# Kernel tuning notes

Hardware: AMD Instinct MI355X
Metric: run time of the kernel (lower is better)

## Reference

```python
import jax, jax.numpy as jnp
import numpy as np

B = 8          # events per batch
NPB = 8192     # points per event (equal counts -> Nmax = NPB)
N = B * NPB
FEAT = 6
K = 128        # max_tokens
TOK = 768      # token_dim
KNN = 16       # k_neighbors
MLP_DIMS = [FEAT, 256, 512, 768, TOK]


def setup_inputs() -> dict:
    key = jax.random.key(0)
    ks = jax.random.split(key, 20)
    coords = jax.random.normal(ks[0], (N, 3), jnp.float32) * 5.0
    features = jax.random.normal(ks[1], (N, FEAT), jnp.float32)
    times = jax.random.uniform(ks[2], (N, 1), jnp.float32)
    # equal-sized, sorted batch ids (8192 points per event)
    batch_ids = jnp.repeat(jnp.arange(B, dtype=jnp.int32), NPB)
    inp = {"coords": coords, "features": features, "batch_ids": batch_ids, "times": times}
    # per-point MLP: 6 -> 256 -> 512 -> 768 -> 768 (last Linear has no ReLU)
    ki = 3
    for i in range(4):
        din, dout = MLP_DIMS[i], MLP_DIMS[i + 1]
        inp[f"W{i+1}"] = jax.random.normal(ks[ki], (din, dout), jnp.float32) / np.sqrt(din); ki += 1
        inp[f"b{i+1}"] = jnp.zeros((dout,), jnp.float32)
    # neighborhood MLP: 768 -> 768 -> 768
    inp["Wn1"] = jax.random.normal(ks[ki], (TOK, TOK), jnp.float32) / np.sqrt(TOK); ki += 1
    inp["bn1"] = jnp.zeros((TOK,), jnp.float32)
    inp["Wn2"] = jax.random.normal(ks[ki], (TOK, TOK), jnp.float32) / np.sqrt(TOK); ki += 1
    inp["bn2"] = jnp.zeros((TOK,), jnp.float32)
    return inp


def _forward(coords, features, batch_ids, times,
             W1, b1, W2, b2, W3, b3, W4, b4, Wn1, bn1, Wn2, bn2):
    INF = jnp.float32(jnp.inf)
    points4 = jnp.concatenate([coords[:, :3], times], axis=-1)  # [N,4] (x,y,z,t)
    # per-point MLP
    h = jax.nn.relu(features @ W1 + b1)
    h = jax.nn.relu(h @ W2 + b2)
    h = jax.nn.relu(h @ W3 + b3)
    feats = h @ W4 + b4                                          # [N,TOK]
    # ---- pack flat -> padded [B, NPB, *] ----
    counts = jnp.bincount(batch_ids, length=B)                   # [B]
    offsets = jnp.cumsum(counts) - counts
    pos = jnp.arange(N) - offsets[batch_ids]
    P = jnp.zeros((B, NPB, 4), points4.dtype).at[batch_ids, pos].set(points4)
    Fp = jnp.zeros((B, NPB, TOK), feats.dtype).at[batch_ids, pos].set(feats)
    valid = jnp.arange(NPB)[None, :] < counts[:, None]           # [B,NPB]
    # ---- small path: take first K points sorted by time ----
    tsort = jnp.where(valid, P[..., 3], INF)
    sorted_idx = jnp.argsort(tsort, axis=1)[:, :K]               # K <= NPB
    tokens_small = jnp.take_along_axis(Fp, sorted_idx[..., None], axis=1)
    cents_small = jnp.take_along_axis(P, sorted_idx[..., None], axis=1)
    masks_small = jnp.arange(K)[None, :] < jnp.minimum(counts, K)[:, None]
    tokens_small = tokens_small * masks_small[..., None]
    cents_small = cents_small * masks_small[..., None]
    # ---- batched FPS over 4D points ----
    min_d0 = jnp.where(valid, INF, 0.0)
    norms = jnp.where(valid, jnp.sum(P * P, axis=-1), -INF)
    first = jnp.argmax(norms, axis=1)                            # farthest-from-origin start
    barange = jnp.arange(B)
    def fps_step(carry, _):
        min_d, last = carry
        c = P[barange, last]                                     # [B,4]
        d = jnp.sum((P - c[:, None, :]) ** 2, axis=-1)
        d = jnp.where(valid, d, INF)
        min_d = jnp.minimum(min_d, d)
        return (min_d, jnp.argmax(min_d, axis=1)), last
    _, idx_seq = jax.lax.scan(fps_step, (min_d0, first), None, length=K)
    fps_idx = idx_seq.T                                          # [B,K]
    validK = jnp.arange(K)[None, :] < jnp.minimum(counts, K)[:, None]
    cents_large = jnp.take_along_axis(P, fps_idx[..., None], axis=1)  # [B,K,4]
    # ---- kNN pooling around centroids ----
    diff = cents_large[:, :, None, :] - P[:, None, :, :]         # [B,K,NPB,4]
    dists = jnp.sum(diff * diff, axis=-1)                        # [B,K,NPB]
    dists = jnp.where(valid[:, None, :], dists, INF)
    k_g = min(KNN, NPB)
    _, knn_idx = jax.lax.top_k(-dists, k_g)                      # smallest-k -> [B,K,k]
    knn_valid = jnp.take_along_axis(jnp.broadcast_to(valid[:, None, :], (B, K, NPB)), knn_idx, axis=2)
    neigh = jnp.take_along_axis(Fp[:, None, :, :], knn_idx[..., None], axis=2)  # [B,K,k,TOK]
    masked = jnp.where(knn_valid[..., None], neigh, -INF)
    pooled = jnp.max(masked, axis=2)
    pooled = jnp.where(jnp.isfinite(pooled), pooled, 0.0)
    tokens_large = jax.nn.relu(pooled @ Wn1 + bn1) @ Wn2 + bn2   # [B,K,TOK]
    # sort selected tokens by centroid time
    ctimes = jnp.where(validK, cents_large[..., 3], INF)
    order = jnp.argsort(ctimes, axis=1)
    tokens_large = jnp.take_along_axis(tokens_large, order[..., None], axis=1)
    cents_large = jnp.take_along_axis(cents_large, order[..., None], axis=1)
    masks_large = jnp.take_along_axis(validK, order, axis=1)
    tokens_large = tokens_large * masks_large[..., None]
    cents_large = cents_large * masks_large[..., None]
    # ---- select per-event path ----
    small = counts <= K
    tokens = jnp.where(small[:, None, None], tokens_small, tokens_large)
    cents = jnp.where(small[:, None, None], cents_small, cents_large)
    masks = jnp.where(small[:, None], masks_small, masks_large)
    return tokens, cents, masks


def reference(coords, features, batch_ids, times,
              W1, b1, W2, b2, W3, b3, W4, b4, Wn1, bn1, Wn2, bn2):
    return _forward(coords, features, batch_ids, times,
                    W1, b1, W2, b2, W3, b3, W4, b4, Wn1, bn1, Wn2, bn2)
```

## Files before the change

### kernel.cpp

```cpp
#include <hip/hip_runtime.h>
#include <hip/hip_bf16.h>


#define BEV 8
#define NPB 8192
#define FEAT 6
#define KTOK 128
#define TOK 768
#define KNN 16

typedef unsigned short ushort_t;
typedef unsigned long long u64;
typedef __bf16 bf16x8 __attribute__((ext_vector_type(8)));
typedef float f32x4 __attribute__((ext_vector_type(4)));
typedef float f32x2 __attribute__((ext_vector_type(2)));

__device__ __forceinline__ ushort_t f2b(float f) {
    union { float f; unsigned int i; } x; x.f = f;
    unsigned int i = x.i;
    unsigned int r = (i + 0x7FFFu + ((i >> 16) & 1u)) >> 16;
    return (ushort_t)r;
}

#define DPP_ROW_SHR1  0x111
#define DPP_ROW_SHR2  0x112
#define DPP_ROW_SHR4  0x114
#define DPP_ROW_SHR8  0x118
#define DPP_ROW_BC15  0x142
#define DPP_ROW_BC31  0x143

template <int CTRL>
__device__ __forceinline__ float dpp_fmax(float v) {
    int o = __builtin_amdgcn_update_dpp(__float_as_int(v), __float_as_int(v),
                                        CTRL, 0xf, 0xf, false);
    return fmaxf(v, __int_as_float(o));
}

template <int CTRL>
__device__ __forceinline__ u64 dpp_u64max(u64 k) {
    int lo = (int)(unsigned)(k & 0xFFFFFFFFu);
    int hi = (int)(unsigned)(k >> 32);
    unsigned olo = (unsigned)__builtin_amdgcn_update_dpp(lo, lo, CTRL, 0xf, 0xf, false);
    unsigned ohi = (unsigned)__builtin_amdgcn_update_dpp(hi, hi, CTRL, 0xf, 0xf, false);
    u64 o = ((u64)ohi << 32) | (u64)olo;
    return o > k ? o : k;
}

__global__ __launch_bounds__(256) void fill_kernel(float* __restrict__ out, int n) {
    int i = blockIdx.x * 256 + threadIdx.x;
    if (i < n) out[i] = 0.f;
}

__global__ __launch_bounds__(1024) void fps_tc(
    const float* __restrict__ coords, const float* __restrict__ times,
    float* __restrict__ cents, int* __restrict__ pos,
    float* __restrict__ cents_out, float* __restrict__ masks_out,
    const float* __restrict__ W2, ushort_t* __restrict__ Wt2,
    const float* __restrict__ W3, ushort_t* __restrict__ Wt3,
    const float* __restrict__ W4, ushort_t* __restrict__ Wt4,
    const float* __restrict__ Wn1, ushort_t* __restrict__ Wn1t,
    const float* __restrict__ Wn2, ushort_t* __restrict__ Wn2t)
{
#pragma clang fp contract(off)
    __shared__ __align__(16) char shmem[137984];
    const int blk = blockIdx.x;
    const int t = threadIdx.x;
    if (blk >= BEV) {
        const int id = (blk - BEV) * 4 + (t >> 8);
        float* tile = (float*)shmem + (t >> 8) * 1056;
        const int tt = t & 255, tx = tt & 31, ty = tt >> 5;
        const float* in; ushort_t* out; int K, N, bx, by;
        if (id < 128)       { in = W2;  out = Wt2;  K = 256; N = 512;
                              bx = id & 15; by = id >> 4; }
        else if (id < 512)  { in = W3;  out = Wt3;  K = 512; N = 768;
                              int r = id - 128;  bx = r % 24; by = r / 24; }
        else if (id < 1088) { in = W4;  out = Wt4;  K = 768; N = 768;
                              int r = id - 512;  bx = r % 24; by = r / 24; }
        else if (id < 1664) { in = Wn1; out = Wn1t; K = 768; N = 768;
                              int r = id - 1088; bx = r % 24; by = r / 24; }
        else                { in = Wn2; out = Wn2t; K = 768; N = 768;
                              int r = id - 1664; bx = r % 24; by = r / 24; }
#pragma unroll
        for (int r = 0; r < 4; ++r) {
            int y = by * 32 + ty + r * 8;
            tile[(ty + r * 8) * 33 + tx] = in[(long)y * N + bx * 32 + tx];
        }
        __syncthreads();
        const int ko = by * 32 + tx;
#pragma unroll
        for (int r = 0; r < 4; ++r) {
            int no = bx * 32 + ty + r * 8;
            out[(long)no * K + ko] = f2b(tile[tx * 33 + ty + r * 8]);
        }
        return;
    }
    float* pts  = (float*)shmem;
    u64*   slotk = (u64*)(shmem + 135168);
    float* tarr = (float*)(shmem + 135424);
    float* carr = (float*)(shmem + 135936);
    const int b = blk;
    f32x2 px[4], py[4], pz[4], pw[4], md[4];
    const long base = (long)b * NPB;
#pragma unroll
    for (int i = 0; i < 4; ++i) {
        long g = base + t * 8 + i * 2;
        px[i] = (f32x2){coords[g * 3 + 0], coords[(g + 1) * 3 + 0]};
        py[i] = (f32x2){coords[g * 3 + 1], coords[(g + 1) * 3 + 1]};
        pz[i] = (f32x2){coords[g * 3 + 2], coords[(g + 1) * 3 + 2]};
        pw[i] = (f32x2){times[g], times[g + 1]};
        md[i] = (f32x2){__builtin_inff(), __builtin_inff()};
    }
#pragma unroll
    for (int i = 0; i < 4; ++i)
#pragma unroll
        for (int e = 0; e < 2; ++e) {
            const int idx = t * 8 + i * 2 + e;
            const int bf = idx * 4 + t;
            pts[bf + 0] = px[i][e]; pts[bf + 1] = py[i][e];
            pts[bf + 2] = pz[i][e]; pts[bf + 3] = pw[i][e];
        }
    const int wv = t >> 6, lane = t & 63;
    float cx = 0.f, cy = 0.f, cz = 0.f, cw = 0.f;
    for (int s = 0; s < KTOK; ++s) {
        f32x2 v[4];
        if (s == 0) {
#pragma unroll
            for (int i = 0; i < 4; ++i)
                v[i] = ((px[i]*px[i] + py[i]*py[i]) + pz[i]*pz[i]) + pw[i]*pw[i];
        } else {
            const f32x2 c2x = {cx, cx}, c2y = {cy, cy}, c2z = {cz, cz}, c2w = {cw, cw};
#pragma unroll
            for (int i = 0; i < 4; ++i) {
                f32x2 dx = px[i] - c2x, dy = py[i] - c2y;
                f32x2 dz = pz[i] - c2z, dw = pw[i] - c2w;
                f32x2 d = ((dx*dx + dy*dy) + dz*dz) + dw*dw;
                md[i] = __builtin_elementwise_min(md[i], d);
                v[i] = md[i];
            }
        }
        f32x2 m01 = __builtin_elementwise_max(v[0], v[1]);
        f32x2 m23 = __builtin_elementwise_max(v[2], v[3]);
        f32x2 mm  = __builtin_elementwise_max(m01, m23);
        const float bv = fmaxf(mm[0], mm[1]);
        float mvv = bv;
        mvv = dpp_fmax<DPP_ROW_SHR1>(mvv);
        mvv = dpp_fmax<DPP_ROW_SHR2>(mvv);
        mvv = dpp_fmax<DPP_ROW_SHR4>(mvv);
        mvv = dpp_fmax<DPP_ROW_SHR8>(mvv);
        mvv = dpp_fmax<DPP_ROW_BC15>(mvv);
        mvv = dpp_fmax<DPP_ROW_BC31>(mvv);
        const float mv = __int_as_float(__builtin_amdgcn_readlane(__float_as_int(mvv), 63));
        const u64 mask = __ballot(bv == mv);
        const int wl = __ffsll((long long)mask) - 1;
        const int p = s & 1;
        if (lane == wl) {
            int bi = t * 8;
#pragma unroll
            for (int j = 7; j >= 0; --j)
                if (v[j >> 1][j & 1] == mv) bi = t * 8 + j;
            slotk[p * 16 + wv] = ((u64)__float_as_uint(mv) << 32)
                               | (unsigned)(NPB - 1 - bi);
        }
        __syncthreads();
        u64 k1 = slotk[p * 16 + (lane & 15)];
        k1 = dpp_u64max<DPP_ROW_SHR1>(k1);
        k1 = dpp_u64max<DPP_ROW_SHR2>(k1);
        k1 = dpp_u64max<DPP_ROW_SHR4>(k1);
        k1 = dpp_u64max<DPP_ROW_SHR8>(k1);
        const unsigned klo =
            (unsigned)__builtin_amdgcn_readlane((int)(unsigned)(k1 & 0xFFFFFFFFu), 15);
        const int widx = NPB - 1 - (int)klo;
        const int bf = widx * 4 + (widx >> 3);
        cx = pts[bf + 0]; cy = pts[bf + 1];
        cz = pts[bf + 2]; cw = pts[bf + 3];
        if (t == 0) {
            tarr[s] = cw;
            carr[s * 4 + 0] = cx; carr[s * 4 + 1] = cy;
            carr[s * 4 + 2] = cz; carr[s * 4 + 3] = cw;
        }
    }
    __syncthreads();
    if (t < KTOK) {
        const float ti = tarr[t];
        int rank = 0;
        for (int j = 0; j < KTOK; ++j) {
            float tj = tarr[j];
            if (tj < ti || (tj == ti && j < t)) ++rank;
        }
        rank &= (KTOK - 1);
        pos[b * KTOK + t] = rank;
        float* cc = &cents[(b * KTOK + t) * 4];
        cc[0] = carr[t * 4 + 0]; cc[1] = carr[t * 4 + 1];
        cc[2] = carr[t * 4 + 2]; cc[3] = carr[t * 4 + 3];
#pragma unroll
        for (int c = 0; c < 4; ++c)
            cents_out[(b * KTOK + rank) * 4 + c] = carr[t * 4 + c];
        masks_out[b * KTOK + t] = 1.0f;
    }
}

__global__ __launch_bounds__(256) void knn_kernel(
    const float* __restrict__ coords, const float* __restrict__ times,
    const float* __restrict__ cents, int* __restrict__ knn_idx)
{
#pragma clang fp contract(off)
    const int blk = blockIdx.x;
    const int b = blk >> 7;
    const int t = threadIdx.x;
    const float cx = cents[blk*4+0], cy = cents[blk*4+1];
    const float cz = cents[blk*4+2], cw = cents[blk*4+3];
    float d[32];
    const long base = (long)b * NPB;
#pragma unroll
    for (int i = 0; i < 32; ++i) {
        long g = base + i * 256 + t;
        float dx = coords[g*3+0] - cx;
        float dy = coords[g*3+1] - cy;
        float dz = coords[g*3+2] - cz;
        float dw = times[g] - cw;
        d[i] = ((dx*dx + dy*dy) + dz*dz) + dw*dw;
    }
    __shared__ float rv[4];
    __shared__ int   ri[4];
    const int wv = t >> 6, lane = t & 63;
    for (int pass = 0; pass < KNN; ++pass) {
        float bvv = __builtin_inff(); int bii = t;
#pragma unroll
        for (int i = 0; i < 32; ++i)
            if (d[i] < bvv) { bvv = d[i]; bii = i * 256 + t; }
        for (int off = 1; off < 64; off <<= 1) {
            float ov = __shfl_xor(bvv, off);
            int   oi = __shfl_xor(bii, off);
            if (ov < bvv || (ov == bvv && oi < bii)) { bvv = ov; bii = oi; }
        }
        if (lane == 0) { rv[wv] = bvv; ri[wv] = bii; }
        __syncthreads();
        float gb = __builtin_inff(); int winner = 0;
        for (int wI = 0; wI < 4; ++wI) {
            float v = rv[wI]; int idx = ri[wI];
            if (v < gb || (v == gb && idx < winner)) { gb = v; winner = idx; }
        }
        winner &= (NPB - 1);
#pragma unroll
        for (int i = 0; i < 32; ++i)
            if (i * 256 + t == winner) d[i] = __builtin_inff();
        if (t == 0) knn_idx[blk * KNN + pass] = winner;
        __syncthreads();
    }
}

#define PAD1 264
#define PAD2 520
#define PAD3 776
__global__ __launch_bounds__(512) void mlp_fused(
    const float* __restrict__ features, const float* __restrict__ W1,
    const float* __restrict__ b1, const int* __restrict__ knn_idx,
    const ushort_t* __restrict__ Wt2, const float* __restrict__ b2,
    const ushort_t* __restrict__ Wt3, const float* __restrict__ b3,
    const ushort_t* __restrict__ Wt4, const float* __restrict__ b4,
    ushort_t* __restrict__ pooled)
{
    __shared__ __align__(16) ushort_t lds[67712];
    ushort_t* h1 = lds;
    ushort_t* h2 = lds + 16896;
    ushort_t* h3 = lds;
    ushort_t* Bs = lds + 50176;
    float*    feat = (float*)(lds + 66560);
    int*      pidx = (int*)(lds + 67584);

    const int bi = blockIdx.x;
    const int t = threadIdx.x;
    const int w = t >> 6, lane = t & 63;
    const int ln = lane & 15, q = lane >> 4;
    const int mg = w >> 2;
    const int wn = w & 3;

    if (t < 64) {
        const int c = bi * 4 + (t >> 4);
        const int ev = c >> 7;
        pidx[t] = ev * NPB + (knn_idx[c * KNN + (t & 15)] & (NPB - 1));
    }
    __syncthreads();
    if (t < 384) {
        const int r = t / 6, f = t - r * 6;
        feat[r * 8 + f] = features[(long)pidx[r] * FEAT + f];
    }
    __syncthreads();
    {
        const int col = t & 255, half = t >> 8;
        float wv[FEAT];
#pragma unroll
        for (int f = 0; f < FEAT; ++f) wv[f] = W1[f * 256 + col];
        const float bias = b1[col];
#pragma unroll
        for (int r = 0; r < 32; ++r) {
            const int row = half * 32 + r;
            float acc = 0.f;
#pragma unroll
            for (int f = 0; f < FEAT; ++f) acc += feat[row * 8 + f] * wv[f];
            h1[row * PAD1 + col] = f2b(fmaxf(acc + bias, 0.f));
        }
    }
    __syncthreads();

    {
        f32x4 acc[2][8];
#pragma unroll
        for (int m = 0; m < 2; ++m)
#pragma unroll
            for (int i = 0; i < 8; ++i) acc[m][i] = (f32x4){0,0,0,0};
        for (int k0 = 0; k0 < 256; k0 += 64) {
            bf16x8 af[2][2];
#pragma unroll
            for (int m = 0; m < 2; ++m)
#pragma unroll
                for (int kh = 0; kh < 2; ++kh)
                    af[m][kh] = *(const bf16x8*)(&h1[(mg * 32 + m * 16 + ln) * PAD1 + k0 + kh * 32 + q * 8]);
#pragma unroll
            for (int np = 0; np < 2; ++np) {
                __syncthreads();
#pragma unroll
                for (int i = 0; i < 4; ++i) {
                    int e = t + i * 512, n = e >> 3, sk = e & 7;
                    *(uint4*)(&Bs[n * 64 + ((sk ^ (n & 7)) * 8)]) =
                        *(const uint4*)(Wt2 + (long)(np * 256 + n) * 256 + k0 + sk * 8);
                }
                __syncthreads();
#pragma unroll
                for (int j = 0; j < 4; ++j) {
                    const int row = (wn * 4 + j) * 16 + ln;
                    bf16x8 bf0 = *(const bf16x8*)(&Bs[row * 64 + ((q ^ (row & 7)) * 8)]);
                    bf16x8 bf1 = *(const bf16x8*)(&Bs[row * 64 + (((4 + q) ^ (row & 7)) * 8)]);
#pragma unroll
                    for (int m = 0; m < 2; ++m) {
                        acc[m][np * 4 + j] = __builtin_amdgcn_mfma_f32_16x16x32_bf16(af[m][0], bf0, acc[m][np * 4 + j], 0, 0, 0);
                        acc[m][np * 4 + j] = __builtin_amdgcn_mfma_f32_16x16x32_bf16(af[m][1], bf1, acc[m][np * 4 + j], 0, 0, 0);
                    }
                }
            }
        }
        __syncthreads();
#pragma unroll
        for (int np = 0; np < 2; ++np)
#pragma unroll
            for (int j = 0; j < 4; ++j) {
                const int col = np * 256 + (wn * 4 + j) * 16 + ln;
                const float bias = b2[col];
#pragma unroll
                for (int m = 0; m < 2; ++m)
#pragma unroll
                    for (int r = 0; r < 4; ++r)
                        h2[(mg * 32 + m * 16 + q * 4 + r) * PAD2 + col] = f2b(fmaxf(acc[m][np * 4 + j][r] + bias, 0.f));
            }
    }
    __syncthreads();

    {
        f32x4 acc[2][12];
#pragma unroll
        for (int m = 0; m < 2; ++m)
#pragma unroll
            for (int i = 0; i < 12; ++i) acc[m][i] = (f32x4){0,0,0,0};
        for (int k0 = 0; k0 < 512; k0 += 64) {
            bf16x8 af[2][2];
#pragma unroll
            for (int m = 0; m < 2; ++m)
#pragma unroll
                for (int kh = 0; kh < 2; ++kh)
                    af[m][kh] = *(const bf16x8*)(&h2[(mg * 32 + m * 16 + ln) * PAD2 + k0 + kh * 32 + q * 8]);
#pragma unroll
            for (int np = 0; np < 3; ++np) {
                __syncthreads();
#pragma unroll
                for (int i = 0; i < 4; ++i) {
                    int e = t + i * 512, n = e >> 3, sk = e & 7;
                    *(uint4*)(&Bs[n * 64 + ((sk ^ (n & 7)) * 8)]) =
                        *(const uint4*)(Wt3 + (long)(np * 256 + n) * 512 + k0 + sk * 8);
                }
                __syncthreads();
#pragma unroll
                for (int j = 0; j < 4; ++j) {
                    const int row = (wn * 4 + j) * 16 + ln;
                    bf16x8 bf0 = *(const bf16x8*)(&Bs[row * 64 + ((q ^ (row & 7)) * 8)]);
                    bf16x8 bf1 = *(const bf16x8*)(&Bs[row * 64 + (((4 + q) ^ (row & 7)) * 8)]);
#pragma unroll
                    for (int m = 0; m < 2; ++m) {
                        acc[m][np * 4 + j] = __builtin_amdgcn_mfma_f32_16x16x32_bf16(af[m][0], bf0, acc[m][np * 4 + j], 0, 0, 0);
                        acc[m][np * 4 + j] = __builtin_amdgcn_mfma_f32_16x16x32_bf16(af[m][1], bf1, acc[m][np * 4 + j], 0, 0, 0);
                    }
                }
            }
        }
        __syncthreads();
#pragma unroll
        for (int np = 0; np < 3; ++np)
#pragma unroll
            for (int j = 0; j < 4; ++j) {
                const int col = np * 256 + (wn * 4 + j) * 16 + ln;
                const float bias = b3[col];
#pragma unroll
                for (int m = 0; m < 2; ++m)
#pragma unroll
                    for (int r = 0; r < 4; ++r)
                        h3[(mg * 32 + m * 16 + q * 4 + r) * PAD3 + col] = f2b(fmaxf(acc[m][np * 4 + j][r] + bias, 0.f));
            }
    }
    __syncthreads();

    {
        f32x4 acc[2][12];
#pragma unroll
        for (int m = 0; m < 2; ++m)
#pragma unroll
            for (int i = 0; i < 12; ++i) acc[m][i] = (f32x4){0,0,0,0};
        for (int k0 = 0; k0 < 768; k0 += 64) {
            bf16x8 af[2][2];
#pragma unroll
            for (int m = 0; m < 2; ++m)
#pragma unroll
                for (int kh = 0; kh < 2; ++kh)
                    af[m][kh] = *(const bf16x8*)(&h3[(mg * 32 + m * 16 + ln) * PAD3 + k0 + kh * 32 + q * 8]);
#pragma unroll
            for (int np = 0; np < 3; ++np) {
                __syncthreads();
#pragma unroll
                for (int i = 0; i < 4; ++i) {
                    int e = t + i * 512, n = e >> 3, sk = e & 7;
                    *(uint4*)(&Bs[n * 64 + ((sk ^ (n & 7)) * 8)]) =
                        *(const uint4*)(Wt4 + (long)(np * 256 + n) * 768 + k0 + sk * 8);
                }
                __syncthreads();
#pragma unroll
                for (int j = 0; j < 4; ++j) {
                    const int row = (wn * 4 + j) * 16 + ln;
                    bf16x8 bf0 = *(const bf16x8*)(&Bs[row * 64 + ((q ^ (row & 7)) * 8)]);
                    bf16x8 bf1 = *(const bf16x8*)(&Bs[row * 64 + (((4 + q) ^ (row & 7)) * 8)]);
#pragma unroll
                    for (int m = 0; m < 2; ++m) {
                        acc[m][np * 4 + j] = __builtin_amdgcn_mfma_f32_16x16x32_bf16(af[m][0], bf0, acc[m][np * 4 + j], 0, 0, 0);
                        acc[m][np * 4 + j] = __builtin_amdgcn_mfma_f32_16x16x32_bf16(af[m][1], bf1, acc[m][np * 4 + j], 0, 0, 0);
                    }
                }
            }
        }
#pragma unroll
        for (int np = 0; np < 3; ++np)
#pragma unroll
            for (int j = 0; j < 4; ++j) {
                const int col = np * 256 + (wn * 4 + j) * 16 + ln;
#pragma unroll
                for (int m = 0; m < 2; ++m) {
                    float v = fmaxf(fmaxf(acc[m][np * 4 + j][0], acc[m][np * 4 + j][1]),
                                    fmaxf(acc[m][np * 4 + j][2], acc[m][np * 4 + j][3]));
                    v = fmaxf(v, __shfl_xor(v, 16));
                    v = fmaxf(v, __shfl_xor(v, 32));
                    if (q == 0)
                        pooled[(long)(bi * 4 + mg * 2 + m) * TOK + col] = f2b(v + b4[col]);
                }
            }
    }
}

template<int EPI, int RELU, int F32OUT, int BT16>
__global__ __launch_bounds__(256) void gemm64_kn(
    const ushort_t* __restrict__ A, const void* __restrict__ Bv,
    const float* __restrict__ bias, void* __restrict__ Cv,
    int M, int N, int Kd, const int* __restrict__ pos)
{
    __shared__ __align__(16) ushort_t As[64 * 40];
    __shared__ __align__(16) ushort_t Bsh[64 * 40];
    const float*    B  = (const float*)Bv;
    const ushort_t* Bt = (const ushort_t*)Bv;
    ushort_t* Cb = (ushort_t*)Cv;
    float*    Cf = (float*)Cv;
    const int tid = threadIdx.x;
    const int m0 = blockIdx.x * 64;
    const int n0 = blockIdx.y * 64;
    const int w = tid >> 6, lane = tid & 63;
    const int ln = lane & 15, q = lane >> 4;
    f32x4 acc[4];
#pragma unroll
    for (int ni = 0; ni < 4; ++ni) acc[ni] = (f32x4){0.f, 0.f, 0.f, 0.f};

    const int ar = tid >> 2, as0 = (tid & 3) * 8;
    const int kk = tid >> 4, nn = (tid & 15) * 4;

    for (int k0 = 0; k0 < Kd; k0 += 32) {
        __syncthreads();
        uint4 a0 = *(const uint4*)(A + (long)(m0 + ar) * Kd + k0 + as0);
        if (BT16) {
            uint4 b0 = *(const uint4*)(Bt + (long)(n0 + ar) * Kd + k0 + as0);
            *(uint4*)(&As[ar * 40 + as0])  = a0;
            *(uint4*)(&Bsh[ar * 40 + as0]) = b0;
        } else {
            float4 f0 = *(const float4*)(B + (long)(k0 + kk)      * N + n0 + nn);
            float4 f1 = *(const float4*)(B + (long)(k0 + kk + 16) * N + n0 + nn);
            *(uint4*)(&As[ar * 40 + as0]) = a0;
            float e0[4] = {f0.x, f0.y, f0.z, f0.w};
            float e1[4] = {f1.x, f1.y, f1.z, f1.w};
#pragma unroll
            for (int j = 0; j < 4; ++j) Bsh[(nn + j) * 40 + kk]      = f2b(e0[j]);
#pragma unroll
            for (int j = 0; j < 4; ++j) Bsh[(nn + j) * 40 + kk + 16] = f2b(e1[j]);
        }
        __syncthreads();
        bf16x8 af = *(const bf16x8*)(&As[(w * 16 + ln) * 40 + q * 8]);
#pragma unroll
        for (int ni = 0; ni < 4; ++ni) {
            bf16x8 bf = *(const bf16x8*)(&Bsh[(ni * 16 + ln) * 40 + q * 8]);
            acc[ni] = __builtin_amdgcn_mfma_f32_16x16x32_bf16(af, bf, acc[ni], 0, 0, 0);
        }
    }

#pragma unroll
    for (int ni = 0; ni < 4; ++ni) {
        const int col = n0 + ni * 16 + ln;
        const float bv = bias[col];
#pragma unroll
        for (int r = 0; r < 4; ++r) {
            const int row = m0 + w * 16 + q * 4 + r;
            float v = acc[ni][r] + bv;
            if (EPI == 0) {
                if (RELU) v = fmaxf(v, 0.f);
                if (F32OUT) Cf[(long)row * N + col] = v;
                else        Cb[(long)row * N + col] = f2b(v);
            } else {
                const int orow = (row & ~(KTOK - 1)) + (pos[row] & (KTOK - 1));
                if (F32OUT) Cf[(long)orow * N + col] = v;
                else        Cb[(long)orow * N + col] = f2b(v);
            }
        }
    }
}

extern "C" void kernel_launch(void* const* d_in, const int* in_sizes, int n_in,
                              void* d_out, int out_size, void* d_ws, size_t ws_size,
                              hipStream_t stream)
{
    const float* coords   = (const float*)d_in[0];
    const float* features = (const float*)d_in[1];
    const float* times    = (const float*)d_in[3];
    const float* W1  = (const float*)d_in[4];
    const float* b1  = (const float*)d_in[5];
    const float* W2  = (const float*)d_in[6];
    const float* b2  = (const float*)d_in[7];
    const float* W3  = (const float*)d_in[8];
    const float* b3  = (const float*)d_in[9];
    const float* W4  = (const float*)d_in[10];
    const float* b4  = (const float*)d_in[11];
    const float* Wn1 = (const float*)d_in[12];
    const float* bn1 = (const float*)d_in[13];
    const float* Wn2 = (const float*)d_in[14];
    const float* bn2 = (const float*)d_in[15];

    char* ws = (char*)d_ws;
    float*    cents   = (float*)(ws + 0);
    int*      pos     = (int*)(ws + 16384);
    int*      knn_idx = (int*)(ws + 20480);
    ushort_t* t1      = (ushort_t*)(ws + 86016);
    ushort_t* pooled  = (ushort_t*)(ws + 1658880);
    ushort_t* Wt2b    = (ushort_t*)(ws + 3231744);
    ushort_t* Wt3b    = (ushort_t*)(ws + 3493888);
    ushort_t* Wt4b    = (ushort_t*)(ws + 4280320);
    ushort_t* Wn1t    = (ushort_t*)(ws + 5459968);
    ushort_t* Wn2t    = (ushort_t*)(ws + 6639616);
    const long WS_NEED = 5459968;
    const long WS_BIG  = 7819264;

    float* tokens_out = (float*)d_out;
    float* cents_out  = tokens_out + 786432;
    float* masks_out  = tokens_out + 790528;

    if ((long)ws_size < WS_NEED) {
        fill_kernel<<<(791552 + 255) / 256, 256, 0, stream>>>(tokens_out, 791552);
        return;
    }
    const bool big = (long)ws_size >= WS_BIG;

    fps_tc<<<BEV + (big ? 560 : 272), 1024, 0, stream>>>(
        coords, times, cents, pos, cents_out, masks_out,
        W2, Wt2b, W3, Wt3b, W4, Wt4b, Wn1, Wn1t, Wn2, Wn2t);

    knn_kernel<<<BEV * KTOK, 256, 0, stream>>>(coords, times, cents, knn_idx);

    mlp_fused<<<256, 512, 0, stream>>>(features, W1, b1, knn_idx,
                                       Wt2b, b2, Wt3b, b3, Wt4b, b4, pooled);

    if (big) {
        gemm64_kn<0,1,0,1><<<dim3(16, 12), 256, 0, stream>>>(pooled, Wn1t, bn1, t1, 1024, 768, 768, nullptr);
        gemm64_kn<2,0,1,1><<<dim3(16, 12), 256, 0, stream>>>(t1, Wn2t, bn2, tokens_out, 1024, 768, 768, pos);
    } else {
        gemm64_kn<0,1,0,0><<<dim3(16, 12), 256, 0, stream>>>(pooled, Wn1, bn1, t1, 1024, 768, 768, nullptr);
        gemm64_kn<2,0,1,0><<<dim3(16, 12), 256, 0, stream>>>(t1, Wn2, bn2, tokens_out, 1024, 768, 768, pos);
    }
}
```

Before: 394.9 us.

## Read MLP weight fragments directly from global memory instead of LDS staging

The fused point-MLP kernel no longer stages each weight tile into shared memory before the MFMA loops. Each wave now loads its bf16 B-fragments straight from global memory (expected to be served from L2), and the loops are reordered to iterate output column groups outermost. This removes two block-wide barriers per tile and shrinks LDS use. In exchange, weight reads become strided per lane and are duplicated across waves. Global-load latency is also no longer hidden behind the shared-memory stage.

```diff
diff --git a/kernel.cpp b/kernel.cpp
--- a/kernel.cpp
+++ b/kernel.cpp
@@ -260,13 +260,12 @@
     const ushort_t* __restrict__ Wt4, const float* __restrict__ b4,
     ushort_t* __restrict__ pooled)
 {
-    __shared__ __align__(16) ushort_t lds[67712];
+    __shared__ __align__(16) ushort_t lds[51328];
     ushort_t* h1 = lds;
     ushort_t* h2 = lds + 16896;
     ushort_t* h3 = lds;
-    ushort_t* Bs = lds + 50176;
-    float*    feat = (float*)(lds + 66560);
-    int*      pidx = (int*)(lds + 67584);
+    float*    feat = (float*)(lds + 50176);
+    int*      pidx = (int*)(lds + 51200);
 
     const int bi = blockIdx.x;
     const int t = threadIdx.x;
@@ -309,28 +308,21 @@
         for (int m = 0; m < 2; ++m)
 #pragma unroll
             for (int i = 0; i < 8; ++i) acc[m][i] = (f32x4){0,0,0,0};
-        for (int k0 = 0; k0 < 256; k0 += 64) {
-            bf16x8 af[2][2];
-#pragma unroll
-            for (int m = 0; m < 2; ++m)
-#pragma unroll
-                for (int kh = 0; kh < 2; ++kh)
-                    af[m][kh] = *(const bf16x8*)(&h1[(mg * 32 + m * 16 + ln) * PAD1 + k0 + kh * 32 + q * 8]);
-#pragma unroll
-            for (int np = 0; np < 2; ++np) {
-                __syncthreads();
-#pragma unroll
-                for (int i = 0; i < 4; ++i) {
-                    int e = t + i * 512, n = e >> 3, sk = e & 7;
-                    *(uint4*)(&Bs[n * 64 + ((sk ^ (n & 7)) * 8)]) =
-                        *(const uint4*)(Wt2 + (long)(np * 256 + n) * 256 + k0 + sk * 8);
-                }
-                __syncthreads();
+#pragma unroll
+        for (int np = 0; np < 2; ++np)
+            for (int k0 = 0; k0 < 256; k0 += 64) {
+                bf16x8 af[2][2];
+#pragma unroll
+                for (int m = 0; m < 2; ++m)
+#pragma unroll
+                    for (int kh = 0; kh < 2; ++kh)
+                        af[m][kh] = *(const bf16x8*)(&h1[(mg * 32 + m * 16 + ln) * PAD1 + k0 + kh * 32 + q * 8]);
 #pragma unroll
                 for (int j = 0; j < 4; ++j) {
                     const int row = (wn * 4 + j) * 16 + ln;
-                    bf16x8 bf0 = *(const bf16x8*)(&Bs[row * 64 + ((q ^ (row & 7)) * 8)]);
-                    bf16x8 bf1 = *(const bf16x8*)(&Bs[row * 64 + (((4 + q) ^ (row & 7)) * 8)]);
+                    const ushort_t* wp = Wt2 + (long)(np * 256 + row) * 256 + k0 + q * 8;
+                    bf16x8 bf0 = *(const bf16x8*)(wp);
+                    bf16x8 bf1 = *(const bf16x8*)(wp + 32);
 #pragma unroll
                     for (int m = 0; m < 2; ++m) {
                         acc[m][np * 4 + j] = __builtin_amdgcn_mfma_f32_16x16x32_bf16(af[m][0], bf0, acc[m][np * 4 + j], 0, 0, 0);
@@ -338,8 +330,6 @@
                     }
                 }
             }
-        }
-        __syncthreads();
 #pragma unroll
         for (int np = 0; np < 2; ++np)
 #pragma unroll
@@ -361,28 +351,21 @@
         for (int m = 0; m < 2; ++m)
 #pragma unroll
             for (int i = 0; i < 12; ++i) acc[m][i] = (f32x4){0,0,0,0};
-        for (int k0 = 0; k0 < 512; k0 += 64) {
-            bf16x8 af[2][2];
-#pragma unroll
-            for (int m = 0; m < 2; ++m)
-#pragma unroll
-                for (int kh = 0; kh < 2; ++kh)
-                    af[m][kh] = *(const bf16x8*)(&h2[(mg * 32 + m * 16 + ln) * PAD2 + k0 + kh * 32 + q * 8]);
-#pragma unroll
-            for (int np = 0; np < 3; ++np) {
-                __syncthreads();
-#pragma unroll
-                for (int i = 0; i < 4; ++i) {
-                    int e = t + i * 512, n = e >> 3, sk = e & 7;
-                    *(uint4*)(&Bs[n * 64 + ((sk ^ (n & 7)) * 8)]) =
-                        *(const uint4*)(Wt3 + (long)(np * 256 + n) * 512 + k0 + sk * 8);
-                }
-                __syncthreads();
+#pragma unroll
+        for (int np = 0; np < 3; ++np)
+            for (int k0 = 0; k0 < 512; k0 += 64) {
+                bf16x8 af[2][2];
+#pragma unroll
+                for (int m = 0; m < 2; ++m)
+#pragma unroll
+                    for (int kh = 0; kh < 2; ++kh)
+                        af[m][kh] = *(const bf16x8*)(&h2[(mg * 32 + m * 16 + ln) * PAD2 + k0 + kh * 32 + q * 8]);
 #pragma unroll
                 for (int j = 0; j < 4; ++j) {
                     const int row = (wn * 4 + j) * 16 + ln;
-                    bf16x8 bf0 = *(const bf16x8*)(&Bs[row * 64 + ((q ^ (row & 7)) * 8)]);
-                    bf16x8 bf1 = *(const bf16x8*)(&Bs[row * 64 + (((4 + q) ^ (row & 7)) * 8)]);
+                    const ushort_t* wp = Wt3 + (long)(np * 256 + row) * 512 + k0 + q * 8;
+                    bf16x8 bf0 = *(const bf16x8*)(wp);
+                    bf16x8 bf1 = *(const bf16x8*)(wp + 32);
 #pragma unroll
                     for (int m = 0; m < 2; ++m) {
                         acc[m][np * 4 + j] = __builtin_amdgcn_mfma_f32_16x16x32_bf16(af[m][0], bf0, acc[m][np * 4 + j], 0, 0, 0);
@@ -390,7 +373,6 @@
                     }
                 }
             }
-        }
         __syncthreads();
 #pragma unroll
         for (int np = 0; np < 3; ++np)
@@ -413,28 +395,21 @@
         for (int m = 0; m < 2; ++m)
 #pragma unroll
             for (int i = 0; i < 12; ++i) acc[m][i] = (f32x4){0,0,0,0};
-        for (int k0 = 0; k0 < 768; k0 += 64) {
-            bf16x8 af[2][2];
-#pragma unroll
-            for (int m = 0; m < 2; ++m)
-#pragma unroll
-                for (int kh = 0; kh < 2; ++kh)
-                    af[m][kh] = *(const bf16x8*)(&h3[(mg * 32 + m * 16 + ln) * PAD3 + k0 + kh * 32 + q * 8]);
-#pragma unroll
-            for (int np = 0; np < 3; ++np) {
-                __syncthreads();
-#pragma unroll
-                for (int i = 0; i < 4; ++i) {
-                    int e = t + i * 512, n = e >> 3, sk = e & 7;
-                    *(uint4*)(&Bs[n * 64 + ((sk ^ (n & 7)) * 8)]) =
-                        *(const uint4*)(Wt4 + (long)(np * 256 + n) * 768 + k0 + sk * 8);
-                }
-                __syncthreads();
+#pragma unroll
+        for (int np = 0; np < 3; ++np)
+            for (int k0 = 0; k0 < 768; k0 += 64) {
+                bf16x8 af[2][2];
+#pragma unroll
+                for (int m = 0; m < 2; ++m)
+#pragma unroll
+                    for (int kh = 0; kh < 2; ++kh)
+                        af[m][kh] = *(const bf16x8*)(&h3[(mg * 32 + m * 16 + ln) * PAD3 + k0 + kh * 32 + q * 8]);
 #pragma unroll
                 for (int j = 0; j < 4; ++j) {
                     const int row = (wn * 4 + j) * 16 + ln;
-                    bf16x8 bf0 = *(const bf16x8*)(&Bs[row * 64 + ((q ^ (row & 7)) * 8)]);
-                    bf16x8 bf1 = *(const bf16x8*)(&Bs[row * 64 + (((4 + q) ^ (row & 7)) * 8)]);
+                    const ushort_t* wp = Wt4 + (long)(np * 256 + row) * 768 + k0 + q * 8;
+                    bf16x8 bf0 = *(const bf16x8*)(wp);
+                    bf16x8 bf1 = *(const bf16x8*)(wp + 32);
 #pragma unroll
                     for (int m = 0; m < 2; ++m) {
                         acc[m][np * 4 + j] = __builtin_amdgcn_mfma_f32_16x16x32_bf16(af[m][0], bf0, acc[m][np * 4 + j], 0, 0, 0);
@@ -442,7 +417,6 @@
                     }
                 }
             }
-        }
 #pragma unroll
         for (int np = 0; np < 3; ++np)
 #pragma unroll
```

New measurement: 463.1 us. +17.3%, slower.
